# Kernel optimization log

Hardware: AMD Instinct MI355X
Metric: run time of the kernel (lower is better)

The kernel has to match this reference:

```python
import jax, jax.numpy as jnp
import numpy as np

N, M, FDIM, EDIM, H, HEADS = 8192, 8192, 128, 128, 64, 4
NEG = -1e9


def setup_inputs() -> dict:
    key = jax.random.key(0)
    ks = jax.random.split(key, 6)
    F0 = jax.random.normal(ks[0], (N, FDIM), dtype=jnp.float32)
    E0 = jax.random.normal(ks[1], (M, EDIM), dtype=jnp.float32)
    A = jax.random.randint(ks[2], (N, M), 0, 2, dtype=jnp.int32)
    Wf = jax.random.normal(ks[3], (HEADS, FDIM, H), dtype=jnp.float32) * 0.05
    We = jax.random.normal(ks[4], (HEADS, EDIM, H), dtype=jnp.float32) * 0.05
    a = jax.random.normal(ks[5], (HEADS, H), dtype=jnp.float32) * 0.05
    return {"F0": F0, "E0": E0, "A": A, "Wf": Wf, "We": We, "a": a}


def reference(F0, E0, A, Wf, We, a):
    # Per-head linear projections: h=head, n/m=nodes, d=hidden
    F1 = jnp.einsum('nf,hfd->hnd', F0, Wf)   # [H, N, D]
    E1 = jnp.einsum('me,hed->hmd', E0, We)   # [H, M, D]
    # Additive GAT scores: (h_src @ a) + (h_dst @ a), broadcast over the grid
    e_src = jnp.einsum('hnd,hd->hn', F1, a)  # [H, N]
    e_dst = jnp.einsum('hmd,hd->hm', E1, a)  # [H, M]
    e = jax.nn.leaky_relu(e_src[:, :, None] + e_dst[:, None, :], negative_slope=0.2)
    e = jnp.where(A[None, :, :] > 0, e, NEG)
    alpha = jax.nn.softmax(e, axis=-1)       # [H, N, M]
    h_prime = jnp.einsum('hnm,hmd->hnd', alpha, E1)  # [H, N, D]
    out = jnp.mean(h_prime, axis=0)          # mean over heads -> [N, D]
    return jax.nn.softmax(out, axis=-1)
```

## Files before the change

### kernel.cpp

```cpp
#include <hip/hip_runtime.h>
#include <hip/hip_fp16.h>

#define NN 8192
#define MM 8192
#define FD 128
#define EDm 128
#define HD 64
#define NH 4
#define NTILE 32
#define BPCOPY 262144

typedef float f32x4 __attribute__((ext_vector_type(4)));
typedef _Float16 h16x8 __attribute__((ext_vector_type(8)));
typedef unsigned int u32;
typedef u32 u32x4 __attribute__((ext_vector_type(4)));

__global__ void k_esrc(const float* __restrict__ F0, const float* __restrict__ Wf,
                       const float* __restrict__ a, float* __restrict__ esrc) {
  __shared__ float vfL[NH * FD];
  int t = threadIdx.x;
#pragma unroll
  for (int r = 0; r < 2; ++r) {
    int idx = t + r * 256;
    int h = idx >> 7, f = idx & 127;
    const float* w = Wf + (size_t)(h * FD + f) * HD;
    const float* av = a + h * HD;
    float s = 0.f;
#pragma unroll
    for (int d = 0; d < HD; ++d) s += w[d] * av[d];
    vfL[idx] = s;
  }
  __syncthreads();
  int g = blockIdx.x * 256 + t;
  int n = g >> 2, h = g & 3;
  const float4* fr = (const float4*)(F0 + (size_t)n * FD);
  const float4* vr = (const float4*)(vfL + h * FD);
  float s = 0.f;
#pragma unroll
  for (int i = 0; i < FD / 4; ++i) {
    float4 x = fr[i], y = vr[i];
    s += x.x * y.x + x.y * y.y + x.z * y.z + x.w * y.w;
  }
  esrc[h * NN + n] = s;
}

__global__ void k_e1(const float* __restrict__ E0, const float* __restrict__ We,
                     const float* __restrict__ a, u32x4* __restrict__ Bp,
                     _Float16* __restrict__ edh, _Float16* __restrict__ ed2h) {
  int wid = (blockIdx.x * blockDim.x + threadIdx.x) >> 6;
  int lane = threadIdx.x & 63;
  int h = wid >> 10;
  int mg = wid & 1023;
  int m = mg * 8;
  const float* we = We + (size_t)h * EDm * HD + lane;
  const float* e0r = E0 + (size_t)m * EDm;
  float ac[8] = {};
#pragma unroll 4
  for (int e = 0; e < EDm; ++e) {
    float wv = we[e * HD];
#pragma unroll
    for (int j = 0; j < 8; ++j) ac[j] += e0r[j * EDm + e] * wv;
  }
  int mc = mg >> 2, quad = mg & 3, dt = lane >> 4, col = lane & 15;
  union { h16x8 v; u32x4 u; } hv;
#pragma unroll
  for (int j = 0; j < 8; ++j) hv.v[j] = (_Float16)ac[j];
  size_t boff = (((size_t)h * 256 + mc) * 4 + dt) * 64 + quad * 16 + col;
#pragma unroll
  for (int c = 0; c < 8; ++c)
    __builtin_nontemporal_store(hv.u, Bp + (size_t)c * BPCOPY + boff);

  float av = a[h * HD + lane];
  float d[8];
#pragma unroll
  for (int j = 0; j < 8; ++j) d[j] = ac[j] * av;
#pragma unroll
  for (int o = 32; o; o >>= 1)
#pragma unroll
    for (int j = 0; j < 8; ++j) d[j] += __shfl_xor(d[j], o);
  if (lane == 0) {
    const float L2E = 1.4426950408889634f;
    union { h16x8 v; u32x4 u; } e1, e2;
#pragma unroll
    for (int j = 0; j < 8; ++j) {
      e1.v[j] = (_Float16)exp2f(d[j] * L2E);
      e2.v[j] = (_Float16)exp2f(0.2f * d[j] * L2E);
    }
    *(u32x4*)(edh + (size_t)h * MM + m) = e1.u;
    *(u32x4*)(ed2h + (size_t)h * MM + m) = e2.u;
  }
}

__device__ __forceinline__ u32 hm2b(u32 w, int bit) {
  return (((w >> bit) & 1u) | (((w >> (bit + 1)) & 1u) << 16)) * 0xffffu;
}

__global__ __launch_bounds__(1024, 4) void k_main(
    const int* __restrict__ A, const u32x4* __restrict__ Bp,
    const float* __restrict__ esrc, const _Float16* __restrict__ edh,
    const _Float16* __restrict__ ed2h, float* __restrict__ out) {
  __shared__ __align__(16) char smem[41472];
  u32* bits = (u32*)smem;
  float* Hsum = (float*)smem;
  float* Dsum = (float*)(smem + 32768);
  float* hp = (float*)(smem + 33280);

  const int t = threadIdx.x;
  const int lane = t & 63;
  const int wv = t >> 6;
  const int h = wv & 3;
  const int q = wv >> 2;
  const int col = lane & 15;
  const int quad = lane >> 4;
  const int qs = quad * 8;
  const int n0 = blockIdx.x * NTILE;
  const float L2E = 1.4426950408889634f;

  {
    const int r0 = wv * 2, r1 = r0 + 1;
    const int* a0p = A + (size_t)(n0 + r0) * MM + lane;
    const int* a1p = A + (size_t)(n0 + r1) * MM + lane;
    for (int c8 = 0; c8 < 16; ++c8) {
      int v0[8], v1[8];
#pragma unroll
      for (int k = 0; k < 8; ++k)
        v0[k] = __builtin_nontemporal_load(a0p + (c8 * 8 + k) * 64);
#pragma unroll
      for (int k = 0; k < 8; ++k)
        v1[k] = __builtin_nontemporal_load(a1p + (c8 * 8 + k) * 64);
#pragma unroll
      for (int k = 0; k < 8; ++k) {
        int c = c8 * 8 + k;
        unsigned long long b = __ballot(v0[k] > 0);
        if (lane == 0) bits[r0 * 257 + 2 * c] = (u32)b;
        if (lane == 32) bits[r0 * 257 + 2 * c + 1] = (u32)(b >> 32);
      }
#pragma unroll
      for (int k = 0; k < 8; ++k) {
        int c = c8 * 8 + k;
        unsigned long long b = __ballot(v1[k] > 0);
        if (lane == 0) bits[r1 * 257 + 2 * c] = (u32)b;
        if (lane == 32) bits[r1 * 257 + 2 * c + 1] = (u32)(b >> 32);
      }
    }
  }
  __syncthreads();

  float s0 = esrc[h * NN + n0 + col];
  float s1 = esrc[h * NN + n0 + 16 + col];
  _Float16 e80 = (_Float16)exp2f(0.8f * s0 * L2E);
  _Float16 e81 = (_Float16)exp2f(0.8f * s1 * L2E);
  h16x8 es80 = {e80, e80, e80, e80, e80, e80, e80, e80};
  h16x8 es81 = {e81, e81, e81, e81, e81, e81, e81, e81};

  f32x4 acc[2][4] = {};
  f32x4 accd[2] = {};
  const h16x8 ones = {(_Float16)1.f, (_Float16)1.f, (_Float16)1.f, (_Float16)1.f,
                      (_Float16)1.f, (_Float16)1.f, (_Float16)1.f, (_Float16)1.f};

  const u32* w0p = bits + col * 257 + q * 64;
  const u32* w1p = bits + (col + 16) * 257 + q * 64;
  const _Float16* edp = edh + (size_t)h * MM + q * 2048 + qs;
  const _Float16* e2p = ed2h + (size_t)h * MM + q * 2048 + qs;
  const u32x4* bp = Bp + (size_t)(blockIdx.x & 7) * BPCOPY +
                    ((size_t)h * 256 + q * 64) * 256 + lane;

  u32 aw0 = w0p[0], aw1 = w1p[0];
  h16x8 edv = *(const h16x8*)edp;
  h16x8 e2v = *(const h16x8*)e2p;
  u32x4 bu0 = bp[0], bu1 = bp[64], bu2 = bp[128], bu3 = bp[192];

#define STEP(PREFETCH)                                                         \
  {                                                                            \
    u32 naw0, naw1;                                                            \
    h16x8 nedv, ne2v;                                                          \
    u32x4 nb0, nb1, nb2, nb3;                                                  \
    if (PREFETCH) {                                                            \
      naw0 = w0p[it + 1];                                                      \
      naw1 = w1p[it + 1];                                                      \
      nedv = *(const h16x8*)(edp + (it + 1) * 32);                             \
      ne2v = *(const h16x8*)(e2p + (it + 1) * 32);                             \
      nb0 = bp[(it + 1) * 256];                                                \
      nb1 = bp[(it + 1) * 256 + 64];                                           \
      nb2 = bp[(it + 1) * 256 + 128];                                          \
      nb3 = bp[(it + 1) * 256 + 192];                                          \
    }                                                                          \
    u32x4 m0, m1;                                                              \
    m0.x = hm2b(aw0, qs);     m0.y = hm2b(aw0, qs + 2);                        \
    m0.z = hm2b(aw0, qs + 4); m0.w = hm2b(aw0, qs + 6);                        \
    m1.x = hm2b(aw1, qs);     m1.y = hm2b(aw1, qs + 2);                        \
    m1.z = hm2b(aw1, qs + 4); m1.w = hm2b(aw1, qs + 6);                        \
    union { h16x8 v; u32x4 u; } w0, w1, b0, b1, b2, b3;                        \
    b0.u = bu0; b1.u = bu1; b2.u = bu2; b3.u = bu3;                            \
    w0.v = __builtin_elementwise_max(edv * es80, e2v);                         \
    w1.v = __builtin_elementwise_max(edv * es81, e2v);                         \
    w0.u &= m0;                                                                \
    w1.u &= m1;                                                                \
    acc[0][0] = __builtin_amdgcn_mfma_f32_16x16x32_f16(w0.v, b0.v, acc[0][0], 0, 0, 0); \
    acc[1][0] = __builtin_amdgcn_mfma_f32_16x16x32_f16(w1.v, b0.v, acc[1][0], 0, 0, 0); \
    acc[0][1] = __builtin_amdgcn_mfma_f32_16x16x32_f16(w0.v, b1.v, acc[0][1], 0, 0, 0); \
    acc[1][1] = __builtin_amdgcn_mfma_f32_16x16x32_f16(w1.v, b1.v, acc[1][1], 0, 0, 0); \
    acc[0][2] = __builtin_amdgcn_mfma_f32_16x16x32_f16(w0.v, b2.v, acc[0][2], 0, 0, 0); \
    acc[1][2] = __builtin_amdgcn_mfma_f32_16x16x32_f16(w1.v, b2.v, acc[1][2], 0, 0, 0); \
    acc[0][3] = __builtin_amdgcn_mfma_f32_16x16x32_f16(w0.v, b3.v, acc[0][3], 0, 0, 0); \
    acc[1][3] = __builtin_amdgcn_mfma_f32_16x16x32_f16(w1.v, b3.v, acc[1][3], 0, 0, 0); \
    accd[0] = __builtin_amdgcn_mfma_f32_16x16x32_f16(w0.v, ones, accd[0], 0, 0, 0);     \
    accd[1] = __builtin_amdgcn_mfma_f32_16x16x32_f16(w1.v, ones, accd[1], 0, 0, 0);     \
    if (PREFETCH) {                                                            \
      aw0 = naw0; aw1 = naw1; edv = nedv; e2v = ne2v;                          \
      bu0 = nb0; bu1 = nb1; bu2 = nb2; bu3 = nb3;                              \
    }                                                                          \
  }

  for (int it = 0; it < 63; ++it) STEP(1)
  {
    const int it = 63;
    (void)it;
    STEP(0)
  }
#undef STEP
  __syncthreads();

  for (int i = t; i < 8320; i += 1024) Hsum[i] = 0.f;
  __syncthreads();

  float* Hh = Hsum + h * 2048;
#pragma unroll
  for (int rt = 0; rt < 2; ++rt) {
#pragma unroll
    for (int dt = 0; dt < 4; ++dt)
#pragma unroll
      for (int r2 = 0; r2 < 4; ++r2)
        atomicAdd(&Hh[(rt * 16 + quad * 4 + r2) * 64 + dt * 16 + col],
                  acc[rt][dt][r2]);
    if (col == 0) {
#pragma unroll
      for (int r2 = 0; r2 < 4; ++r2)
        atomicAdd(&Dsum[h * 32 + rt * 16 + quad * 4 + r2], accd[rt][r2]);
    }
  }
  __syncthreads();

  for (int i = t; i < 2048; i += 1024) {
    int r = i >> 6;
    float v = 0.f;
#pragma unroll
    for (int hh = 0; hh < 4; ++hh) v += Hsum[hh * 2048 + i] / Dsum[hh * 32 + r];
    hp[i] = 0.25f * v;
  }
  __syncthreads();

#pragma unroll
  for (int i = 0; i < 2; ++i) {
    int r = wv * 2 + i;
    float v = hp[r * 64 + lane];
    float mx = v;
#pragma unroll
    for (int o = 32; o; o >>= 1) mx = fmaxf(mx, __shfl_xor(mx, o));
    float p = exp2f((v - mx) * L2E);
    float sm = p;
#pragma unroll
    for (int o = 32; o; o >>= 1) sm += __shfl_xor(sm, o);
    out[(size_t)(n0 + r) * HD + lane] = p / sm;
  }
}

extern "C" void kernel_launch(void* const* d_in, const int* in_sizes, int n_in,
                              void* d_out, int out_size, void* d_ws, size_t ws_size,
                              hipStream_t stream) {
  const float* F0 = (const float*)d_in[0];
  const float* E0 = (const float*)d_in[1];
  const int* A = (const int*)d_in[2];
  const float* Wf = (const float*)d_in[3];
  const float* We = (const float*)d_in[4];
  const float* a = (const float*)d_in[5];
  float* out = (float*)d_out;

  char* w = (char*)d_ws;
  float* esrc = (float*)w;        w += (size_t)NH * NN * 4;
  _Float16* edh = (_Float16*)w;   w += (size_t)NH * MM * 2;
  _Float16* ed2h = (_Float16*)w;  w += (size_t)NH * MM * 2;
  u32x4* Bp = (u32x4*)w;          w += (size_t)8 * BPCOPY * 16;

  k_esrc<<<(NH * NN) / 256 / 4, 256, 0, stream>>>(F0, Wf, a, esrc);
  k_e1<<<(NH * MM / 8) / 4, 256, 0, stream>>>(E0, We, a, Bp, edh, ed2h);
  k_main<<<NN / NTILE, 1024, 0, stream>>>(A, Bp, esrc, edh, ed2h, out);
}
```

Measured before the change: 502.9 us.

## Drop replicated B copies and deepen main-loop prefetch to three stages

The projection kernel now writes a single packed fp16 copy of E1 instead of eight nontemporal replicas, and the main kernel reads that one copy from every block. The main loop changes from one-step register prefetch to a three-deep rotating software pipeline over mask, edge-score and B loads. The launch-bounds occupancy hint of 4 is removed. This cuts write traffic in the projection kernel and hides more load latency, at the cost of more registers and possible contention on the shared copy.

```diff
diff --git a/kernel.cpp b/kernel.cpp
--- a/kernel.cpp
+++ b/kernel.cpp
@@ -8,7 +8,6 @@
 #define HD 64
 #define NH 4
 #define NTILE 32
-#define BPCOPY 262144
 
 typedef float f32x4 __attribute__((ext_vector_type(4)));
 typedef _Float16 h16x8 __attribute__((ext_vector_type(8)));
@@ -65,10 +64,7 @@
   union { h16x8 v; u32x4 u; } hv;
 #pragma unroll
   for (int j = 0; j < 8; ++j) hv.v[j] = (_Float16)ac[j];
-  size_t boff = (((size_t)h * 256 + mc) * 4 + dt) * 64 + quad * 16 + col;
-#pragma unroll
-  for (int c = 0; c < 8; ++c)
-    __builtin_nontemporal_store(hv.u, Bp + (size_t)c * BPCOPY + boff);
+  Bp[(((size_t)h * 256 + mc) * 4 + dt) * 64 + quad * 16 + col] = hv.u;
 
   float av = a[h * HD + lane];
   float d[8];
@@ -95,7 +91,7 @@
   return (((w >> bit) & 1u) | (((w >> (bit + 1)) & 1u) << 16)) * 0xffffu;
 }
 
-__global__ __launch_bounds__(1024, 4) void k_main(
+__global__ __launch_bounds__(1024) void k_main(
     const int* __restrict__ A, const u32x4* __restrict__ Bp,
     const float* __restrict__ esrc, const _Float16* __restrict__ edh,
     const _Float16* __restrict__ ed2h, float* __restrict__ out) {
@@ -162,38 +158,35 @@
   const u32* w1p = bits + (col + 16) * 257 + q * 64;
   const _Float16* edp = edh + (size_t)h * MM + q * 2048 + qs;
   const _Float16* e2p = ed2h + (size_t)h * MM + q * 2048 + qs;
-  const u32x4* bp = Bp + (size_t)(blockIdx.x & 7) * BPCOPY +
-                    ((size_t)h * 256 + q * 64) * 256 + lane;
-
-  u32 aw0 = w0p[0], aw1 = w1p[0];
-  h16x8 edv = *(const h16x8*)edp;
-  h16x8 e2v = *(const h16x8*)e2p;
-  u32x4 bu0 = bp[0], bu1 = bp[64], bu2 = bp[128], bu3 = bp[192];
-
-#define STEP(PREFETCH)                                                         \
+  const u32x4* bp = Bp + ((size_t)h * 256 + q * 64) * 256 + lane;
+
+  u32 saw0[3], saw1[3];
+  h16x8 sed[3], se2[3];
+  u32x4 sb0[3], sb1[3], sb2[3], sb3[3];
+
+#define PRELOAD(S, ITV)                                                        \
   {                                                                            \
-    u32 naw0, naw1;                                                            \
-    h16x8 nedv, ne2v;                                                          \
-    u32x4 nb0, nb1, nb2, nb3;                                                  \
-    if (PREFETCH) {                                                            \
-      naw0 = w0p[it + 1];                                                      \
-      naw1 = w1p[it + 1];                                                      \
-      nedv = *(const h16x8*)(edp + (it + 1) * 32);                             \
-      ne2v = *(const h16x8*)(e2p + (it + 1) * 32);                             \
-      nb0 = bp[(it + 1) * 256];                                                \
-      nb1 = bp[(it + 1) * 256 + 64];                                           \
-      nb2 = bp[(it + 1) * 256 + 128];                                          \
-      nb3 = bp[(it + 1) * 256 + 192];                                          \
-    }                                                                          \
+    saw0[S] = w0p[ITV];                                                        \
+    saw1[S] = w1p[ITV];                                                        \
+    sed[S] = *(const h16x8*)(edp + (ITV) * 32);                                \
+    se2[S] = *(const h16x8*)(e2p + (ITV) * 32);                                \
+    sb0[S] = bp[(ITV) * 256];                                                  \
+    sb1[S] = bp[(ITV) * 256 + 64];                                             \
+    sb2[S] = bp[(ITV) * 256 + 128];                                            \
+    sb3[S] = bp[(ITV) * 256 + 192];                                            \
+  }
+
+#define BODY(S, ITV, PF)                                                       \
+  {                                                                            \
     u32x4 m0, m1;                                                              \
-    m0.x = hm2b(aw0, qs);     m0.y = hm2b(aw0, qs + 2);                        \
-    m0.z = hm2b(aw0, qs + 4); m0.w = hm2b(aw0, qs + 6);                        \
-    m1.x = hm2b(aw1, qs);     m1.y = hm2b(aw1, qs + 2);                        \
-    m1.z = hm2b(aw1, qs + 4); m1.w = hm2b(aw1, qs + 6);                        \
+    m0.x = hm2b(saw0[S], qs);     m0.y = hm2b(saw0[S], qs + 2);                \
+    m0.z = hm2b(saw0[S], qs + 4); m0.w = hm2b(saw0[S], qs + 6);                \
+    m1.x = hm2b(saw1[S], qs);     m1.y = hm2b(saw1[S], qs + 2);                \
+    m1.z = hm2b(saw1[S], qs + 4); m1.w = hm2b(saw1[S], qs + 6);                \
     union { h16x8 v; u32x4 u; } w0, w1, b0, b1, b2, b3;                        \
-    b0.u = bu0; b1.u = bu1; b2.u = bu2; b3.u = bu3;                            \
-    w0.v = __builtin_elementwise_max(edv * es80, e2v);                         \
-    w1.v = __builtin_elementwise_max(edv * es81, e2v);                         \
+    b0.u = sb0[S]; b1.u = sb1[S]; b2.u = sb2[S]; b3.u = sb3[S];                \
+    w0.v = __builtin_elementwise_max(sed[S] * es80, se2[S]);                   \
+    w1.v = __builtin_elementwise_max(sed[S] * es81, se2[S]);                   \
     w0.u &= m0;                                                                \
     w1.u &= m1;                                                                \
     acc[0][0] = __builtin_amdgcn_mfma_f32_16x16x32_f16(w0.v, b0.v, acc[0][0], 0, 0, 0); \
@@ -206,19 +199,21 @@
     acc[1][3] = __builtin_amdgcn_mfma_f32_16x16x32_f16(w1.v, b3.v, acc[1][3], 0, 0, 0); \
     accd[0] = __builtin_amdgcn_mfma_f32_16x16x32_f16(w0.v, ones, accd[0], 0, 0, 0);     \
     accd[1] = __builtin_amdgcn_mfma_f32_16x16x32_f16(w1.v, ones, accd[1], 0, 0, 0);     \
-    if (PREFETCH) {                                                            \
-      aw0 = naw0; aw1 = naw1; edv = nedv; e2v = ne2v;                          \
-      bu0 = nb0; bu1 = nb1; bu2 = nb2; bu3 = nb3;                              \
-    }                                                                          \
-  }
-
-  for (int it = 0; it < 63; ++it) STEP(1)
-  {
-    const int it = 63;
-    (void)it;
-    STEP(0)
-  }
-#undef STEP
+    if (PF) PRELOAD(S, (ITV) + 3)                                              \
+  }
+
+  PRELOAD(0, 0)
+  PRELOAD(1, 1)
+  PRELOAD(2, 2)
+
+  for (int itb = 0; itb < 63; itb += 3) {
+    BODY(0, itb, itb + 3 < 64)
+    BODY(1, itb + 1, itb + 4 < 64)
+    BODY(2, itb + 2, itb + 5 < 64)
+  }
+  BODY(0, 63, 0)
+#undef BODY
+#undef PRELOAD
   __syncthreads();
 
   for (int i = t; i < 8320; i += 1024) Hsum[i] = 0.f;
@@ -280,7 +275,7 @@
   float* esrc = (float*)w;        w += (size_t)NH * NN * 4;
   _Float16* edh = (_Float16*)w;   w += (size_t)NH * MM * 2;
   _Float16* ed2h = (_Float16*)w;  w += (size_t)NH * MM * 2;
-  u32x4* Bp = (u32x4*)w;          w += (size_t)8 * BPCOPY * 16;
+  u32x4* Bp = (u32x4*)w;          w += (size_t)NH * HD * MM * 2;
 
   k_esrc<<<(NH * NN) / 256 / 4, 256, 0, stream>>>(F0, Wf, a, esrc);
   k_e1<<<(NH * MM / 8) / 4, 256, 0, stream>>>(E0, We, a, Bp, edh, ed2h);
```

New measurement: 943.5 us. 87.6% more time.
